# Kernel optimization log

Measured on AMD Instinct MI355X. Metric: run time of the kernel, lower is better.

The kernel has to match this reference:

```python
import jax, jax.numpy as jnp
import numpy as np

B, D_MODEL, N_LAYERS = 8, 512, 4
D_STATE, D_CONV, EXPAND, DT_RANK = 16, 4, 2, 32
D_INNER = EXPAND * D_MODEL
NUM_CLASSES = 10
ALPHA = 0.2  # observer_alpha
LN_EPS = 1e-5


def setup_inputs() -> dict:
    key = jax.random.key(0)
    ks = jax.random.split(key, 10)
    std = 0.02
    rn = lambda k, sh: (jax.random.normal(k, sh) * std).astype(jnp.float32)
    return {
        "x": jax.random.normal(ks[0], (B, 3, 32, 32), dtype=jnp.float32),
        "W_inp": rn(ks[1], (3, D_MODEL)), "b_inp": jnp.zeros((D_MODEL,), jnp.float32),
        "W_in": rn(ks[2], (N_LAYERS, D_MODEL, 2 * D_INNER)), "b_in": jnp.zeros((N_LAYERS, 2 * D_INNER), jnp.float32),
        "conv_w": rn(ks[3], (N_LAYERS, D_INNER, D_CONV)), "conv_b": jnp.zeros((N_LAYERS, D_INNER), jnp.float32),
        "W_x": rn(ks[4], (N_LAYERS, D_INNER, DT_RANK + 2 * D_STATE)),
        "W_dt": rn(ks[5], (N_LAYERS, DT_RANK, D_INNER)), "b_dt": jnp.zeros((N_LAYERS, D_INNER), jnp.float32),
        "A_log": jnp.broadcast_to(jnp.log(jnp.arange(1, D_STATE + 1, dtype=jnp.float32)), (N_LAYERS, D_INNER, D_STATE)) + 0.0,
        "D_skip": jnp.ones((N_LAYERS, D_INNER), jnp.float32),
        "W_out": rn(ks[6], (N_LAYERS, D_INNER, D_MODEL)), "b_out": jnp.zeros((N_LAYERS, D_MODEL), jnp.float32),
        "ln_w": jnp.ones((N_LAYERS, D_MODEL), jnp.float32), "ln_b": jnp.zeros((N_LAYERS, D_MODEL), jnp.float32),
        "lnf_w": jnp.ones((D_MODEL,), jnp.float32), "lnf_b": jnp.zeros((D_MODEL,), jnp.float32),
        "W_cls": rn(ks[7], (D_MODEL, NUM_CLASSES)), "b_cls": jnp.zeros((NUM_CLASSES,), jnp.float32),
    }


def layernorm(x, w, b):
    mu = x.mean(-1, keepdims=True)
    var = jnp.mean(jnp.square(x - mu), -1, keepdims=True)
    return (x - mu) * jax.lax.rsqrt(var + LN_EPS) * w + b


def mamba_layer(x, Wi, bi, cw, cb, Wx, Wdt, bdt, Alog, Dv, Wo, bo):
    # x: [B, L, d_model]
    Bsz, L, _ = x.shape
    u, z = jnp.split(x @ Wi + bi, 2, axis=-1)  # each [B, L, d_inner]
    # causal depthwise conv1d, kernel width D_CONV
    up = jnp.pad(u, ((0, 0), (D_CONV - 1, 0), (0, 0)))
    uc = cb + sum(up[:, k:k + L, :] * cw[:, k] for k in range(D_CONV))
    uc = jax.nn.silu(uc)
    dbc = uc @ Wx  # [B, L, dt_rank + 2*d_state]
    dt = jax.nn.softplus(dbc[..., :DT_RANK] @ Wdt + bdt)       # [B, L, d_inner]
    Bm = dbc[..., DT_RANK:DT_RANK + D_STATE]                    # [B, L, d_state]
    Cm = dbc[..., DT_RANK + D_STATE:]                           # [B, L, d_state]
    A = -jnp.exp(Alog)                                          # [d_inner, d_state]

    def step(h, inp):
        u_t, dt_t, B_t, C_t = inp  # [B,E],[B,E],[B,N],[B,N]
        h = jnp.exp(dt_t[..., None] * A) * h + (dt_t * u_t)[..., None] * B_t[:, None, :]
        # Luenberger observer correction: h <- h + alpha * (u - C.h) * C^T
        err = u_t - jnp.einsum('ben,bn->be', h, C_t)
        h = h + ALPHA * err[..., None] * C_t[:, None, :]
        y = jnp.einsum('ben,bn->be', h, C_t)
        return h, y

    step = jax.checkpoint(step)
    h0 = jnp.zeros((Bsz, D_INNER, D_STATE), dtype=x.dtype)
    xs = (uc.transpose(1, 0, 2), dt.transpose(1, 0, 2), Bm.transpose(1, 0, 2), Cm.transpose(1, 0, 2))
    _, ys = jax.lax.scan(step, h0, xs)
    y = ys.transpose(1, 0, 2) + Dv * uc
    y = y * jax.nn.silu(z)
    return y @ Wo + bo


def reference(x, W_inp, b_inp, W_in, b_in, conv_w, conv_b, W_x, W_dt, b_dt, A_log, D_skip, W_out, b_out, ln_w, ln_b, lnf_w, lnf_b, W_cls, b_cls):
    Bsz = x.shape[0]
    t = x.transpose(0, 2, 3, 1).reshape(Bsz, -1, 3)  # [B, H*W, 3]
    t = t @ W_inp + b_inp                             # [B, L, d_model]
    for i in range(N_LAYERS):
        t = t + mamba_layer(layernorm(t, ln_w[i], ln_b[i]), W_in[i], b_in[i], conv_w[i], conv_b[i], W_x[i], W_dt[i], b_dt[i], A_log[i], D_skip[i], W_out[i], b_out[i])
    t = t.mean(axis=1)
    t = layernorm(t, lnf_w, lnf_b)
    return t @ W_cls + b_cls
```

## Files before the change

### kernel.cpp

```cpp
#include <hip/hip_runtime.h>
#include <hip/hip_bf16.h>
#include <math.h>

#define BSZ 8
#define SEQL 1024
#define DM 512
#define DI 1024
#define DST 16
#define DTR 32
#define NLAYERS 4
#define ALPHA_C 0.2f
#define LNEPS 1e-5f
#define CH 64
#define KS64 8
#define YSTR 18

typedef __attribute__((ext_vector_type(8))) short short8;
typedef __attribute__((ext_vector_type(4))) float f32x4;

__device__ __forceinline__ void gll16(const void* g, void* l) {
    __builtin_amdgcn_global_load_lds(
        (const __attribute__((address_space(1))) unsigned int*)g,
        (__attribute__((address_space(3))) unsigned int*)l, 16, 0, 0);
}

__device__ __forceinline__ float sum16(float x) {
    x += __int_as_float(__builtin_amdgcn_update_dpp(0, __float_as_int(x), 0x121, 0xf, 0xf, true));
    x += __int_as_float(__builtin_amdgcn_update_dpp(0, __float_as_int(x), 0x122, 0xf, 0xf, true));
    x += __int_as_float(__builtin_amdgcn_update_dpp(0, __float_as_int(x), 0x124, 0xf, 0xf, true));
    x += __int_as_float(__builtin_amdgcn_update_dpp(0, __float_as_int(x), 0x128, 0xf, 0xf, true));
    return x;
}

__device__ __forceinline__ float bf2f(unsigned short v) {
    return __uint_as_float(((unsigned)v) << 16);
}

__global__ __launch_bounds__(256) void embed_kernel(const float* __restrict__ x,
                                                    const float* __restrict__ Wi,
                                                    const float* __restrict__ bi,
                                                    float* __restrict__ t) {
    int idx = blockIdx.x * 256 + threadIdx.x;
    if (idx >= BSZ * SEQL * DM) return;
    int d  = idx & (DM - 1);
    int bl = idx >> 9;
    int l  = bl & (SEQL - 1);
    int b  = bl >> 10;
    const float* xb = x + (size_t)b * 3 * SEQL;
    float acc = bi[d];
    acc += xb[0 * SEQL + l] * Wi[0 * DM + d];
    acc += xb[1 * SEQL + l] * Wi[1 * DM + d];
    acc += xb[2 * SEQL + l] * Wi[2 * DM + d];
    t[idx] = acc;
}

__global__ __launch_bounds__(256) void ln_kernel(const float* __restrict__ t,
                                                 const float* __restrict__ w,
                                                 const float* __restrict__ b,
                                                 __hip_bfloat16* __restrict__ xn) {
    int row = blockIdx.x;
    int tid = threadIdx.x;
    const float* r = t + (size_t)row * DM;
    float v0 = r[tid], v1 = r[tid + 256];
    __shared__ float sh[256], sh2[256];
    sh[tid]  = v0 + v1;
    sh2[tid] = v0 * v0 + v1 * v1;
    __syncthreads();
    for (int off = 128; off > 0; off >>= 1) {
        if (tid < off) { sh[tid] += sh[tid + off]; sh2[tid] += sh2[tid + off]; }
        __syncthreads();
    }
    float mu  = sh[0]  * (1.f / DM);
    float var = sh2[0] * (1.f / DM) - mu * mu;
    float rs  = rsqrtf(var + LNEPS);
    xn[(size_t)row * DM + tid]       = __float2bfloat16((v0 - mu) * rs * w[tid]       + b[tid]);
    xn[(size_t)row * DM + tid + 256] = __float2bfloat16((v1 - mu) * rs * w[tid + 256] + b[tid + 256]);
}

__global__ __launch_bounds__(256) void transpose_bf_kernel(const float* __restrict__ W,
                                                           __hip_bfloat16* __restrict__ Wt,
                                                           int K, int N, size_t lstride) {
    const float* Wl = W + (size_t)blockIdx.z * lstride;
    __hip_bfloat16* Wtl = Wt + (size_t)blockIdx.z * lstride;
    __shared__ float tile[32][33];
    int kk = blockIdx.x * 32, nn = blockIdx.y * 32;
    int tx = threadIdx.x & 31, ty = threadIdx.x >> 5;
#pragma unroll
    for (int i = 0; i < 32; i += 8)
        tile[ty + i][tx] = Wl[(size_t)(kk + ty + i) * N + nn + tx];
    __syncthreads();
#pragma unroll
    for (int i = 0; i < 32; i += 8)
        Wtl[(size_t)(nn + ty + i) * K + kk + tx] = __float2bfloat16(tile[tx][ty + i]);
}

template <int OUTMODE>
__global__ __launch_bounds__(256) void gemm_mfma_kernel(const short* __restrict__ A,
                                                        const short* __restrict__ Bt,
                                                        const float* __restrict__ bias,
                                                        void* __restrict__ Cv,
                                                        int M, int N, int K) {
    __shared__ __align__(16) short As[128 * 64];
    __shared__ __align__(16) short Bs[128 * 64];
    int tid = threadIdx.x;
    int w = tid >> 6, lane = tid & 63;
    int quad = lane >> 4, ml = lane & 15;
    int wm = w & 1, wn = w >> 1;
    const short* Ab = A + (size_t)blockIdx.x * 128 * K;
    const short* Bb = Bt + (size_t)blockIdx.y * 128 * K;
    f32x4 acc[4][4] = {};
    int rS[4], cS[4];
#pragma unroll
    for (int i = 0; i < 4; i++) {
        int s = i * 256 + tid;
        rS[i] = s >> 3;
        cS[i] = (s & 7) ^ (rS[i] & 7);
    }
    int aoff[2][4], boff[2][4];
#pragma unroll
    for (int kc = 0; kc < 2; kc++)
#pragma unroll
        for (int t = 0; t < 4; t++) {
            int ra = wm * 64 + t * 16 + ml;
            aoff[kc][t] = ra * 64 + ((kc * 4 + quad) ^ (ra & 7)) * 8;
            int rb = wn * 64 + t * 16 + ml;
            boff[kc][t] = rb * 64 + ((kc * 4 + quad) ^ (rb & 7)) * 8;
        }
    for (int kk = 0; kk < K; kk += 64) {
#pragma unroll
        for (int i = 0; i < 4; i++) {
            gll16(Ab + (size_t)rS[i] * K + kk + cS[i] * 8, As + (size_t)(i * 256 + w * 64) * 8);
            gll16(Bb + (size_t)rS[i] * K + kk + cS[i] * 8, Bs + (size_t)(i * 256 + w * 64) * 8);
        }
        __syncthreads();
#pragma unroll
        for (int kc = 0; kc < 2; kc++) {
            short8 af[4], bfr[4];
#pragma unroll
            for (int t = 0; t < 4; t++) af[t]  = *(const short8*)&As[aoff[kc][t]];
#pragma unroll
            for (int t = 0; t < 4; t++) bfr[t] = *(const short8*)&Bs[boff[kc][t]];
#pragma unroll
            for (int mt = 0; mt < 4; mt++)
#pragma unroll
                for (int nt = 0; nt < 4; nt++)
                    acc[mt][nt] = __builtin_amdgcn_mfma_f32_16x16x32_bf16(af[mt], bfr[nt], acc[mt][nt], 0, 0, 0);
        }
        __syncthreads();
    }
#pragma unroll
    for (int mt = 0; mt < 4; mt++) {
#pragma unroll
        for (int nt = 0; nt < 4; nt++) {
            int n = blockIdx.y * 128 + wn * 64 + nt * 16 + ml;
            float bv = bias[n];
#pragma unroll
            for (int r = 0; r < 4; r++) {
                int m = blockIdx.x * 128 + wm * 64 + mt * 16 + quad * 4 + r;
                size_t off = (size_t)m * N + n;
                float v = acc[mt][nt][r] + bv;
                if (OUTMODE == 2) {
                    ((unsigned short*)Cv)[off] = __bfloat16_as_ushort(__float2bfloat16(v));
                } else {
                    float* C = (float*)Cv;
                    if (OUTMODE == 1) v += C[off];
                    C[off] = v;
                }
            }
        }
    }
}

__global__ __launch_bounds__(256) void gemm6464_res_kernel(const short* __restrict__ A,
                                                           const short* __restrict__ Bt,
                                                           const float* __restrict__ bias,
                                                           float* __restrict__ C,
                                                           int M, int N, int K) {
    __shared__ __align__(16) short As[64 * 64];
    __shared__ __align__(16) short Bs[64 * 64];
    int tid = threadIdx.x;
    int w = tid >> 6, lane = tid & 63;
    int quad = lane >> 4, ml = lane & 15;
    int wm = w & 1, wn = w >> 1;
    const short* Ab = A + (size_t)blockIdx.x * 64 * K;
    const short* Bb = Bt + (size_t)blockIdx.y * 64 * K;
    f32x4 acc[2][2] = {};
    int rS[2], cS[2];
#pragma unroll
    for (int i = 0; i < 2; i++) {
        int s = i * 256 + tid;
        rS[i] = s >> 3;
        cS[i] = (s & 7) ^ (rS[i] & 7);
    }
    int aoff[2][2], boff[2][2];
#pragma unroll
    for (int kc = 0; kc < 2; kc++)
#pragma unroll
        for (int t = 0; t < 2; t++) {
            int ra = wm * 32 + t * 16 + ml;
            aoff[kc][t] = ra * 64 + ((kc * 4 + quad) ^ (ra & 7)) * 8;
            int rb = wn * 32 + t * 16 + ml;
            boff[kc][t] = rb * 64 + ((kc * 4 + quad) ^ (rb & 7)) * 8;
        }
    for (int kk = 0; kk < K; kk += 64) {
#pragma unroll
        for (int i = 0; i < 2; i++) {
            gll16(Ab + (size_t)rS[i] * K + kk + cS[i] * 8, As + (size_t)(i * 256 + w * 64) * 8);
            gll16(Bb + (size_t)rS[i] * K + kk + cS[i] * 8, Bs + (size_t)(i * 256 + w * 64) * 8);
        }
        __syncthreads();
#pragma unroll
        for (int kc = 0; kc < 2; kc++) {
            short8 af[2], bfr[2];
#pragma unroll
            for (int t = 0; t < 2; t++) af[t]  = *(const short8*)&As[aoff[kc][t]];
#pragma unroll
            for (int t = 0; t < 2; t++) bfr[t] = *(const short8*)&Bs[boff[kc][t]];
#pragma unroll
            for (int mt = 0; mt < 2; mt++)
#pragma unroll
                for (int nt = 0; nt < 2; nt++)
                    acc[mt][nt] = __builtin_amdgcn_mfma_f32_16x16x32_bf16(af[mt], bfr[nt], acc[mt][nt], 0, 0, 0);
        }
        __syncthreads();
    }
#pragma unroll
    for (int mt = 0; mt < 2; mt++) {
#pragma unroll
        for (int nt = 0; nt < 2; nt++) {
            int n = blockIdx.y * 64 + wn * 32 + nt * 16 + ml;
            float bv = bias[n];
#pragma unroll
            for (int r = 0; r < 4; r++) {
                int m = blockIdx.x * 64 + wm * 32 + mt * 16 + quad * 4 + r;
                size_t off = (size_t)m * N + n;
                C[off] = acc[mt][nt][r] + bv + C[off];
            }
        }
    }
}

__global__ __launch_bounds__(256) void conv_kernel(const unsigned short* __restrict__ uzb,
                                                   const float* __restrict__ cw,
                                                   const float* __restrict__ cb,
                                                   unsigned short* __restrict__ ucb) {
    int idx = blockIdx.x * 256 + threadIdx.x;
    int e  = idx & (DI - 1);
    int bl = idx >> 10;
    int l  = bl & (SEQL - 1);
    int b  = bl >> 10;
    const unsigned short* u = uzb + (size_t)b * SEQL * 2048;
    float acc = cb[e];
#pragma unroll
    for (int k = 0; k < 4; k++) {
        int ll = l - 3 + k;
        float uv = (ll >= 0) ? bf2f(u[(size_t)ll * 2048 + e]) : 0.f;
        acc += uv * cw[e * 4 + k];
    }
    acc = acc / (1.f + __expf(-acc));
    ucb[idx] = __bfloat16_as_ushort(__float2bfloat16(acc));
}

__global__ __launch_bounds__(256) void gemm64_mfma_kernel(const short* __restrict__ A,
                                                          const short* __restrict__ Bt,
                                                          float* __restrict__ part,
                                                          int M) {
    const int K = DI;
    const int Kseg = K / KS64;
    __shared__ __align__(16) short As[128 * 32];
    __shared__ __align__(16) short Bs[64 * 32];
    int tid = threadIdx.x;
    int w = tid >> 6, lane = tid & 63;
    int quad = lane >> 4, ml = lane & 15;
    int wm = w & 1, wn = w >> 1;
    int bm = blockIdx.x, ks = blockIdx.y;
    const short* Ab = A + (size_t)bm * 128 * K;
    f32x4 acc[4][2] = {};
    int s0 = tid, s1 = tid + 256;
    int r0 = s0 >> 2, c0 = (s0 & 3) ^ ((r0 >> 1) & 3);
    int r1 = s1 >> 2, c1 = (s1 & 3) ^ ((r1 >> 1) & 3);
    int rB = tid >> 2, cB = (tid & 3) ^ ((rB >> 1) & 3);
    int aoff[4], boff[2];
#pragma unroll
    for (int t = 0; t < 4; t++) {
        int ra = wm * 64 + t * 16 + ml;
        aoff[t] = ra * 32 + (quad ^ ((ra >> 1) & 3)) * 8;
    }
#pragma unroll
    for (int t = 0; t < 2; t++) {
        int rb = wn * 32 + t * 16 + ml;
        boff[t] = rb * 32 + (quad ^ ((rb >> 1) & 3)) * 8;
    }
    int k0 = ks * Kseg;
    for (int kk = k0; kk < k0 + Kseg; kk += 32) {
        gll16(Ab + (size_t)r0 * K + kk + c0 * 8, As + (size_t)(w * 64) * 8);
        gll16(Ab + (size_t)r1 * K + kk + c1 * 8, As + (size_t)(256 + w * 64) * 8);
        gll16(Bt + (size_t)rB * K + kk + cB * 8, Bs + (size_t)(w * 64) * 8);
        __syncthreads();
        short8 af[4], bfr[2];
#pragma unroll
        for (int t = 0; t < 4; t++) af[t]  = *(const short8*)&As[aoff[t]];
#pragma unroll
        for (int t = 0; t < 2; t++) bfr[t] = *(const short8*)&Bs[boff[t]];
#pragma unroll
        for (int mt = 0; mt < 4; mt++)
#pragma unroll
            for (int nt = 0; nt < 2; nt++)
                acc[mt][nt] = __builtin_amdgcn_mfma_f32_16x16x32_bf16(af[mt], bfr[nt], acc[mt][nt], 0, 0, 0);
        __syncthreads();
    }
#pragma unroll
    for (int mt = 0; mt < 4; mt++) {
#pragma unroll
        for (int nt = 0; nt < 2; nt++) {
            int n = wn * 32 + nt * 16 + ml;
#pragma unroll
            for (int r = 0; r < 4; r++) {
                int m = bm * 128 + wm * 64 + mt * 16 + quad * 4 + r;
                part[((size_t)ks * M + m) * 64 + n] = acc[mt][nt][r];
            }
        }
    }
}

__global__ __launch_bounds__(256) void dt_kernel(const float* __restrict__ part,
                                                 const float* __restrict__ Wdt,
                                                 const float* __restrict__ bdt,
                                                 const unsigned short* __restrict__ ucb,
                                                 unsigned* __restrict__ dub,
                                                 unsigned* __restrict__ bcb,
                                                 float* __restrict__ ssqb,
                                                 int M) {
    __shared__ float sdtc[32][32];
    __shared__ float swdt[32][256];
    int tid = threadIdx.x;
    int e0 = (blockIdx.x & 3) * 256;
    int m0 = (blockIdx.x >> 2) * 32;
#pragma unroll
    for (int i = 0; i < 4; i++) {
        int idx = tid + 256 * i;
        int m = idx >> 5, r = idx & 31;
        float v = 0.f;
#pragma unroll
        for (int ks = 0; ks < KS64; ks++) v += part[((size_t)ks * M + m0 + m) * 64 + r];
        sdtc[m][r] = v;
    }
    if ((blockIdx.x & 3) == 0) {
#pragma unroll
        for (int i = 0; i < 4; i++) {
            int idx = tid + 256 * i;
            int m = m0 + (idx >> 5);
            int j = idx & 31;
            float v = 0.f;
#pragma unroll
            for (int ks = 0; ks < KS64; ks++) v += part[((size_t)ks * M + m) * 64 + 32 + j];
            int n = j & 15;
            unsigned short u16 = __bfloat16_as_ushort(__float2bfloat16(v));
            unsigned short* bp = (unsigned short*)(bcb + (size_t)m * 16 + n);
            if (j < 16) {
                bp[0] = u16;
            } else {
                bp[1] = u16;
                float vr = bf2f(u16);
                float s = sum16(vr * vr);
                if (j == 16) ssqb[m] = s;
            }
        }
    }
#pragma unroll
    for (int r = 0; r < 32; r++) swdt[r][tid] = Wdt[(size_t)r * DI + e0 + tid];
    __syncthreads();
    float wc[32];
#pragma unroll
    for (int r = 0; r < 32; r++) wc[r] = swdt[r][tid];
    float bv = bdt[e0 + tid];
    for (int m = 0; m < 32; m++) {
        float acc = bv;
#pragma unroll
        for (int r4 = 0; r4 < 8; r4++) {
            float4 d4 = *(const float4*)&sdtc[m][r4 * 4];
            acc = fmaf(d4.x, wc[r4 * 4 + 0], acc);
            acc = fmaf(d4.y, wc[r4 * 4 + 1], acc);
            acc = fmaf(d4.z, wc[r4 * 4 + 2], acc);
            acc = fmaf(d4.w, wc[r4 * 4 + 3], acc);
        }
        float sp = (acc > 20.f) ? acc : log1pf(__expf(acc));
        unsigned dt16 = (unsigned)__bfloat16_as_ushort(__float2bfloat16(sp));
        unsigned u16  = (unsigned)ucb[(size_t)(m0 + m) * DI + e0 + tid];
        dub[(size_t)(m0 + m) * DI + e0 + tid] = (dt16 << 16) | u16;
    }
}

__device__ __forceinline__ void scan_stage(unsigned* sDU, unsigned* sBC,
                                           const unsigned* __restrict__ dub_row,
                                           const unsigned* __restrict__ bcb_row,
                                           int e_base, int tid, int tc) {
    int w = tid >> 6;
    int t4 = tid >> 2, c4 = tid & 3;
    gll16(dub_row + (size_t)(tc + t4) * 1024 + e_base + c4 * 4, sDU + w * 256);
    gll16(bcb_row + (size_t)(tc + t4) * 16 + c4 * 4,            sBC + w * 256);
}

__device__ __forceinline__ void scan_flush(const float* yb, __hip_bfloat16* ob,
                                           int e_base, int tcp, int tid) {
#pragma unroll
    for (int r = 0; r < 2; r++) {
        int pid = r * 256 + tid;
        int t = pid >> 3, ep = pid & 7;
        float2 y2 = *(const float2*)&yb[t * YSTR + ep * 2];
        __hip_bfloat162 v;
        v.x = __float2bfloat16(y2.x);
        v.y = __float2bfloat16(y2.y);
        *(__hip_bfloat162*)&ob[(size_t)(tcp + t) * DI + e_base + ep * 2] = v;
    }
}

__global__ __launch_bounds__(256, 2) void scan_kernel(const unsigned* __restrict__ dub,
                                                      const unsigned short* __restrict__ uzb,
                                                      const unsigned* __restrict__ bcb,
                                                      const float* __restrict__ ssqb,
                                                      const float* __restrict__ Alog,
                                                      const float* __restrict__ Dv,
                                                      __hip_bfloat16* __restrict__ out) {
    __shared__ __align__(16) unsigned sDU[2][CH * 16];
    __shared__ __align__(16) unsigned sBC[2][CH * 16];
    __shared__ __align__(16) float    yb [2][CH * YSTR];
    int tid = threadIdx.x;
    int g = tid >> 4, n = tid & 15;
    int b = blockIdx.x >> 6;
    int e_base = (blockIdx.x & 63) << 4;
    int e = e_base + g;
    float An2 = -__expf(Alog[e * DST + n]) * 1.4426950408889634f;
    float dv = Dv[e];
    const unsigned*       dub_row = dub + (size_t)b * SEQL * DI;
    const unsigned short* zP      = uzb + (size_t)b * SEQL * 2048 + 1024 + e;
    const unsigned*       bcb_row = bcb + (size_t)b * SEQL * 16;
    const float*          sqP     = ssqb + (size_t)b * SEQL;
    __hip_bfloat16* ob = out + (size_t)b * SEQL * DI;
    float h = 0.f;
    scan_stage(sDU[0], sBC[0], dub_row, bcb_row, e_base, tid, 0);
    int buf = 0;
    for (int c = 0; c < SEQL / CH; c++) {
        int tc = c * CH;
        __syncthreads();
        if (c + 1 < SEQL / CH)
            scan_stage(sDU[buf ^ 1], sBC[buf ^ 1], dub_row, bcb_row, e_base, tid, tc + CH);
        if (c > 0)
            scan_flush(yb[buf ^ 1], ob, e_base, tc - CH, tid);
        const unsigned* pDU = sDU[buf];
        const unsigned* pBC = sBC[buf];
        float* pY = yb[buf];
        for (int ts = 0; ts < CH; ts += 16) {
            unsigned du16[16], bc16[16];
#pragma unroll
            for (int j = 0; j < 16; j++) {
                du16[j] = pDU[(ts + j) * 16 + g];
                bc16[j] = pBC[(ts + j) * 16 + n];
            }
            int tl = ts + n;
            float sq = sqP[tc + tl];
            float zv = bf2f(zP[(size_t)(tc + tl) * 2048]);
            float pc = 0.f, ucap = 0.f;
#pragma unroll
            for (int j = 0; j < 16; j++) {
                unsigned du = du16[j];
                float dtv = __uint_as_float(du & 0xFFFF0000u);
                float uv  = __uint_as_float(du << 16);
                unsigned bcd = bc16[j];
                float Bn = __uint_as_float(bcd << 16);
                float Cn = __uint_as_float(bcd & 0xFFFF0000u);
                float a = __builtin_amdgcn_exp2f(dtv * An2);
                h = fmaf(a, h, dtv * uv * Bn);
                float p = sum16(h * Cn);
                h = fmaf(uv - p, ALPHA_C * Cn, h);
                bool cap = (n == j);
                pc   = cap ? p  : pc;
                ucap = cap ? uv : ucap;
            }
            float es2 = ALPHA_C * (ucap - pc);
            float y = fmaf(dv, ucap, fmaf(es2, sq, pc));
            float sz = zv / (1.f + __expf(-zv));
            pY[tl * YSTR + g] = y * sz;
        }
        buf ^= 1;
    }
    __syncthreads();
    scan_flush(yb[buf ^ 1], ob, e_base, SEQL - CH, tid);
}

__global__ __launch_bounds__(512) void pool_kernel(const float* __restrict__ t,
                                                   float* __restrict__ part) {
    int b = blockIdx.x >> 4;
    int c = blockIdx.x & 15;
    int d = threadIdx.x;
    const float* tb = t + ((size_t)b * SEQL + c * 64) * DM + d;
    float s = 0.f;
    for (int l = 0; l < 64; l++) s += tb[(size_t)l * DM];
    part[(size_t)blockIdx.x * DM + d] = s;
}

__global__ __launch_bounds__(512) void final_kernel(const float* __restrict__ part,
                                                    const float* __restrict__ lw,
                                                    const float* __restrict__ lb,
                                                    const float* __restrict__ Wc,
                                                    const float* __restrict__ bc,
                                                    float* __restrict__ out) {
    int b = blockIdx.x;
    int d = threadIdx.x;
    float v = 0.f;
    for (int c = 0; c < 16; c++) v += part[((size_t)b * 16 + c) * DM + d];
    v *= (1.f / SEQL);
    __shared__ float sh[512], sh2[512], nd[512];
    sh[d] = v; sh2[d] = v * v;
    __syncthreads();
    for (int off = 256; off > 0; off >>= 1) {
        if (d < off) { sh[d] += sh[d + off]; sh2[d] += sh2[d + off]; }
        __syncthreads();
    }
    float mu  = sh[0]  * (1.f / DM);
    float var = sh2[0] * (1.f / DM) - mu * mu;
    float rs  = rsqrtf(var + LNEPS);
    nd[d] = (v - mu) * rs * lw[d] + lb[d];
    __syncthreads();
    if (d < 10) {
        float acc = bc[d];
        for (int k = 0; k < DM; k++) acc += nd[k] * Wc[k * 10 + d];
        out[b * 10 + d] = acc;
    }
}

extern "C" void kernel_launch(void* const* d_in, const int* in_sizes, int n_in,
                              void* d_out, int out_size, void* d_ws, size_t ws_size,
                              hipStream_t stream) {
    const float* x      = (const float*)d_in[0];
    const float* W_inp  = (const float*)d_in[1];
    const float* b_inp  = (const float*)d_in[2];
    const float* W_in   = (const float*)d_in[3];
    const float* b_in   = (const float*)d_in[4];
    const float* conv_w = (const float*)d_in[5];
    const float* conv_b = (const float*)d_in[6];
    const float* W_x    = (const float*)d_in[7];
    const float* W_dt   = (const float*)d_in[8];
    const float* b_dt   = (const float*)d_in[9];
    const float* A_log  = (const float*)d_in[10];
    const float* D_skip = (const float*)d_in[11];
    const float* W_out  = (const float*)d_in[12];
    const float* b_out  = (const float*)d_in[13];
    const float* ln_w   = (const float*)d_in[14];
    const float* ln_b   = (const float*)d_in[15];
    const float* lnf_w  = (const float*)d_in[16];
    const float* lnf_b  = (const float*)d_in[17];
    const float* W_cls  = (const float*)d_in[18];
    const float* b_cls  = (const float*)d_in[19];

    const int M = BSZ * SEQL;

    float* ws = (float*)d_ws;
    float* t_buf = ws;                          ws += (size_t)M * DM;
    unsigned short* uzb = (unsigned short*)ws;  ws += (size_t)M * 2048 / 2;
    unsigned short* ucb = (unsigned short*)ws;  ws += (size_t)M * DI / 2;
    unsigned* dub  = (unsigned*)ws;             ws += (size_t)M * DI;
    unsigned* bcbu = (unsigned*)ws;             ws += (size_t)M * 16;
    float* ssqb  = ws;                          ws += (size_t)M;
    unsigned short* xn_bf = (unsigned short*)ws;  ws += (size_t)M * DM / 2;
    unsigned short* ucs_bf = (unsigned short*)ws; ws += (size_t)M * DI / 2;
    float* partb = ws;                          ws += (size_t)KS64 * M * 64;
    unsigned short* wtin_bf  = (unsigned short*)ws; ws += (size_t)NLAYERS * DM * 2048 / 2;
    unsigned short* wtout_bf = (unsigned short*)ws; ws += (size_t)NLAYERS * DI * DM / 2;
    unsigned short* wxt_bf   = (unsigned short*)ws; ws += (size_t)NLAYERS * DI * 64 / 2 + 64;
    float* poolp = ws;                          ws += (size_t)128 * DM;

    embed_kernel<<<(M * DM + 255) / 256, 256, 0, stream>>>(x, W_inp, b_inp, t_buf);
    transpose_bf_kernel<<<dim3(DM / 32, 2048 / 32, NLAYERS), 256, 0, stream>>>(
        W_in, (__hip_bfloat16*)wtin_bf, DM, 2048, (size_t)DM * 2048);
    transpose_bf_kernel<<<dim3(DI / 32, DM / 32, NLAYERS), 256, 0, stream>>>(
        W_out, (__hip_bfloat16*)wtout_bf, DI, DM, (size_t)DI * DM);
    transpose_bf_kernel<<<dim3(DI / 32, 64 / 32, NLAYERS), 256, 0, stream>>>(
        W_x, (__hip_bfloat16*)wxt_bf, DI, 64, (size_t)DI * 64);

    for (int i = 0; i < NLAYERS; i++) {
        ln_kernel<<<M, 256, 0, stream>>>(t_buf, ln_w + i * DM, ln_b + i * DM,
                                         (__hip_bfloat16*)xn_bf);
        gemm_mfma_kernel<2><<<dim3(M / 128, 2048 / 128), 256, 0, stream>>>(
            (const short*)xn_bf, (const short*)(wtin_bf + (size_t)i * DM * 2048),
            b_in + i * 2048, uzb, M, 2048, DM);
        conv_kernel<<<(M * DI) / 256, 256, 0, stream>>>(
            uzb, conv_w + (size_t)i * DI * 4, conv_b + i * DI, ucb);
        gemm64_mfma_kernel<<<dim3(M / 128, KS64), 256, 0, stream>>>(
            (const short*)ucb, (const short*)(wxt_bf + (size_t)i * DI * 64), partb, M);
        dt_kernel<<<(M / 32) * 4, 256, 0, stream>>>(
            partb, W_dt + (size_t)i * DTR * DI, b_dt + i * DI, ucb, dub, bcbu, ssqb, M);
        scan_kernel<<<BSZ * DI / 16, 256, 0, stream>>>(
            dub, uzb, bcbu, ssqb, A_log + (size_t)i * DI * DST, D_skip + i * DI,
            (__hip_bfloat16*)ucs_bf);
        gemm6464_res_kernel<<<dim3(M / 64, DM / 64), 256, 0, stream>>>(
            (const short*)ucs_bf, (const short*)(wtout_bf + (size_t)i * DI * DM),
            b_out + i * DM, t_buf, M, DM, DI);
    }

    pool_kernel<<<128, 512, 0, stream>>>(t_buf, poolp);
    final_kernel<<<8, 512, 0, stream>>>(poolp, lnf_w, lnf_b, W_cls, b_cls, (float*)d_out);
}
```

Baseline: 1.147 ms.

## Transpose dt/u and B/C buffers to time-major per channel for vectorized scan loads

The dt kernel now writes the packed dt/u and B/C values transposed, so each channel's (or state's) time series is contiguous. The scan kernel then loads them with register-staged uint4 global loads into padded shared rows instead of global_load_lds. It also reads four timesteps per uint4 from shared memory with software prefetch, replacing sixteen scalar reads. The cost is that the dt kernel's column writes become strided across channels, which may hurt its store coalescing.

New measurement: 1.387 ms. 1.21x slower.

```diff
diff --git a/kernel.cpp b/kernel.cpp
--- a/kernel.cpp
+++ b/kernel.cpp
@@ -14,6 +14,7 @@
 #define CH 64
 #define KS64 8
 #define YSTR 18
+#define SROW 68
 
 typedef __attribute__((ext_vector_type(8))) short short8;
 typedef __attribute__((ext_vector_type(4))) float f32x4;
@@ -327,8 +328,8 @@
                                                  const float* __restrict__ Wdt,
                                                  const float* __restrict__ bdt,
                                                  const unsigned short* __restrict__ ucb,
-                                                 unsigned* __restrict__ dub,
-                                                 unsigned* __restrict__ bcb,
+                                                 unsigned* __restrict__ dub_t,
+                                                 unsigned* __restrict__ bcb_t,
                                                  float* __restrict__ ssqb,
                                                  int M) {
     __shared__ float sdtc[32][32];
@@ -336,6 +337,8 @@
     int tid = threadIdx.x;
     int e0 = (blockIdx.x & 3) * 256;
     int m0 = (blockIdx.x >> 2) * 32;
+    int mb = m0 >> 10;
+    int t0 = m0 & 1023;
 #pragma unroll
     for (int i = 0; i < 4; i++) {
         int idx = tid + 256 * i;
@@ -355,8 +358,9 @@
 #pragma unroll
             for (int ks = 0; ks < KS64; ks++) v += part[((size_t)ks * M + m) * 64 + 32 + j];
             int n = j & 15;
+            int tt = m & 1023;
             unsigned short u16 = __bfloat16_as_ushort(__float2bfloat16(v));
-            unsigned short* bp = (unsigned short*)(bcb + (size_t)m * 16 + n);
+            unsigned short* bp = (unsigned short*)(bcb_t + ((size_t)mb * 16 + n) * SEQL + tt);
             if (j < 16) {
                 bp[0] = u16;
             } else {
@@ -374,6 +378,7 @@
 #pragma unroll
     for (int r = 0; r < 32; r++) wc[r] = swdt[r][tid];
     float bv = bdt[e0 + tid];
+    unsigned* dcol = dub_t + ((size_t)mb * DI + e0 + tid) * SEQL + t0;
     for (int m = 0; m < 32; m++) {
         float acc = bv;
 #pragma unroll
@@ -387,18 +392,8 @@
         float sp = (acc > 20.f) ? acc : log1pf(__expf(acc));
         unsigned dt16 = (unsigned)__bfloat16_as_ushort(__float2bfloat16(sp));
         unsigned u16  = (unsigned)ucb[(size_t)(m0 + m) * DI + e0 + tid];
-        dub[(size_t)(m0 + m) * DI + e0 + tid] = (dt16 << 16) | u16;
-    }
-}
-
-__device__ __forceinline__ void scan_stage(unsigned* sDU, unsigned* sBC,
-                                           const unsigned* __restrict__ dub_row,
-                                           const unsigned* __restrict__ bcb_row,
-                                           int e_base, int tid, int tc) {
-    int w = tid >> 6;
-    int t4 = tid >> 2, c4 = tid & 3;
-    gll16(dub_row + (size_t)(tc + t4) * 1024 + e_base + c4 * 4, sDU + w * 256);
-    gll16(bcb_row + (size_t)(tc + t4) * 16 + c4 * 4,            sBC + w * 256);
+        dcol[m] = (dt16 << 16) | u16;
+    }
 }
 
 __device__ __forceinline__ void scan_flush(const float* yb, __hip_bfloat16* ob,
@@ -415,15 +410,15 @@
     }
 }
 
-__global__ __launch_bounds__(256, 2) void scan_kernel(const unsigned* __restrict__ dub,
+__global__ __launch_bounds__(256, 2) void scan_kernel(const unsigned* __restrict__ dub_t,
                                                       const unsigned short* __restrict__ uzb,
-                                                      const unsigned* __restrict__ bcb,
+                                                      const unsigned* __restrict__ bcb_t,
                                                       const float* __restrict__ ssqb,
                                                       const float* __restrict__ Alog,
                                                       const float* __restrict__ Dv,
                                                       __hip_bfloat16* __restrict__ out) {
-    __shared__ __align__(16) unsigned sDU[2][CH * 16];
-    __shared__ __align__(16) unsigned sBC[2][CH * 16];
+    __shared__ __align__(16) unsigned sDU[2][16 * SROW];
+    __shared__ __align__(16) unsigned sBC[2][16 * SROW];
     __shared__ __align__(16) float    yb [2][CH * YSTR];
     int tid = threadIdx.x;
     int g = tid >> 4, n = tid & 15;
@@ -432,55 +427,82 @@
     int e = e_base + g;
     float An2 = -__expf(Alog[e * DST + n]) * 1.4426950408889634f;
     float dv = Dv[e];
-    const unsigned*       dub_row = dub + (size_t)b * SEQL * DI;
-    const unsigned short* zP      = uzb + (size_t)b * SEQL * 2048 + 1024 + e;
-    const unsigned*       bcb_row = bcb + (size_t)b * SEQL * 16;
-    const float*          sqP     = ssqb + (size_t)b * SEQL;
+    int er = tid >> 4, tq = (tid & 15) * 4;
+    const unsigned* duRow = dub_t + ((size_t)b * DI + e_base + er) * SEQL + tq;
+    const unsigned* bcRow = bcb_t + ((size_t)b * 16 + er) * SEQL + tq;
+    int dst = er * SROW + tq;
+    const unsigned short* zP  = uzb + (size_t)b * SEQL * 2048 + 1024 + e;
+    const float*          sqP = ssqb + (size_t)b * SEQL;
     __hip_bfloat16* ob = out + (size_t)b * SEQL * DI;
     float h = 0.f;
-    scan_stage(sDU[0], sBC[0], dub_row, bcb_row, e_base, tid, 0);
+    {
+        uint4 a = *(const uint4*)(duRow);
+        uint4 c = *(const uint4*)(bcRow);
+        *(uint4*)&sDU[0][dst] = a;
+        *(uint4*)&sBC[0][dst] = c;
+    }
     int buf = 0;
-    for (int c = 0; c < SEQL / CH; c++) {
+    const int NCH = SEQL / CH;
+    for (int c = 0; c < NCH; c++) {
         int tc = c * CH;
         __syncthreads();
-        if (c + 1 < SEQL / CH)
-            scan_stage(sDU[buf ^ 1], sBC[buf ^ 1], dub_row, bcb_row, e_base, tid, tc + CH);
+        uint4 gdu, gbc;
+        bool more = (c + 1 < NCH);
+        if (more) {
+            gdu = *(const uint4*)(duRow + tc + CH);
+            gbc = *(const uint4*)(bcRow + tc + CH);
+        }
         if (c > 0)
             scan_flush(yb[buf ^ 1], ob, e_base, tc - CH, tid);
-        const unsigned* pDU = sDU[buf];
-        const unsigned* pBC = sBC[buf];
+        const unsigned* pDU = &sDU[buf][g * SROW];
+        const unsigned* pBC = &sBC[buf][n * SROW];
         float* pY = yb[buf];
-        for (int ts = 0; ts < CH; ts += 16) {
-            unsigned du16[16], bc16[16];
-#pragma unroll
-            for (int j = 0; j < 16; j++) {
-                du16[j] = pDU[(ts + j) * 16 + g];
-                bc16[j] = pBC[(ts + j) * 16 + n];
-            }
-            int tl = ts + n;
-            float sq = sqP[tc + tl];
-            float zv = bf2f(zP[(size_t)(tc + tl) * 2048]);
-            float pc = 0.f, ucap = 0.f;
-#pragma unroll
-            for (int j = 0; j < 16; j++) {
-                unsigned du = du16[j];
+        uint4 du4 = *(const uint4*)&pDU[0];
+        uint4 bc4 = *(const uint4*)&pBC[0];
+        float pc = 0.f, ucap = 0.f, sq = 0.f, zv = 0.f;
+#pragma unroll
+        for (int p = 0; p < 16; p++) {
+            uint4 duN, bcN;
+            if (p < 15) {
+                duN = *(const uint4*)&pDU[(p + 1) * 4];
+                bcN = *(const uint4*)&pBC[(p + 1) * 4];
+            }
+            if ((p & 3) == 0) {
+                int tl = (p >> 2) * 16 + n;
+                sq = sqP[tc + tl];
+                zv = bf2f(zP[(size_t)(tc + tl) * 2048]);
+                pc = 0.f; ucap = 0.f;
+            }
+            unsigned dus[4] = {du4.x, du4.y, du4.z, du4.w};
+            unsigned bcs[4] = {bc4.x, bc4.y, bc4.z, bc4.w};
+#pragma unroll
+            for (int j = 0; j < 4; j++) {
+                unsigned du = dus[j];
                 float dtv = __uint_as_float(du & 0xFFFF0000u);
                 float uv  = __uint_as_float(du << 16);
-                unsigned bcd = bc16[j];
+                unsigned bcd = bcs[j];
                 float Bn = __uint_as_float(bcd << 16);
                 float Cn = __uint_as_float(bcd & 0xFFFF0000u);
                 float a = __builtin_amdgcn_exp2f(dtv * An2);
                 h = fmaf(a, h, dtv * uv * Bn);
-                float p = sum16(h * Cn);
-                h = fmaf(uv - p, ALPHA_C * Cn, h);
-                bool cap = (n == j);
-                pc   = cap ? p  : pc;
+                float p2 = sum16(h * Cn);
+                h = fmaf(uv - p2, ALPHA_C * Cn, h);
+                bool cap = (n == ((p & 3) * 4 + j));
+                pc   = cap ? p2 : pc;
                 ucap = cap ? uv : ucap;
             }
-            float es2 = ALPHA_C * (ucap - pc);
-            float y = fmaf(dv, ucap, fmaf(es2, sq, pc));
-            float sz = zv / (1.f + __expf(-zv));
-            pY[tl * YSTR + g] = y * sz;
+            if ((p & 3) == 3) {
+                int tl = (p >> 2) * 16 + n;
+                float es2 = ALPHA_C * (ucap - pc);
+                float y = fmaf(dv, ucap, fmaf(es2, sq, pc));
+                float sz = zv / (1.f + __expf(-zv));
+                pY[tl * YSTR + g] = y * sz;
+            }
+            du4 = duN; bc4 = bcN;
+        }
+        if (more) {
+            *(uint4*)&sDU[buf ^ 1][dst] = gdu;
+            *(uint4*)&sBC[buf ^ 1][dst] = gbc;
         }
         buf ^= 1;
     }
@@ -559,8 +581,8 @@
     float* t_buf = ws;                          ws += (size_t)M * DM;
     unsigned short* uzb = (unsigned short*)ws;  ws += (size_t)M * 2048 / 2;
     unsigned short* ucb = (unsigned short*)ws;  ws += (size_t)M * DI / 2;
-    unsigned* dub  = (unsigned*)ws;             ws += (size_t)M * DI;
-    unsigned* bcbu = (unsigned*)ws;             ws += (size_t)M * 16;
+    unsigned* dub_t = (unsigned*)ws;            ws += (size_t)M * DI;
+    unsigned* bcb_t = (unsigned*)ws;            ws += (size_t)BSZ * 16 * SEQL;
     float* ssqb  = ws;                          ws += (size_t)M;
     unsigned short* xn_bf = (unsigned short*)ws;  ws += (size_t)M * DM / 2;
     unsigned short* ucs_bf = (unsigned short*)ws; ws += (size_t)M * DI / 2;
@@ -589,9 +611,9 @@
         gemm64_mfma_kernel<<<dim3(M / 128, KS64), 256, 0, stream>>>(
             (const short*)ucb, (const short*)(wxt_bf + (size_t)i * DI * 64), partb, M);
         dt_kernel<<<(M / 32) * 4, 256, 0, stream>>>(
-            partb, W_dt + (size_t)i * DTR * DI, b_dt + i * DI, ucb, dub, bcbu, ssqb, M);
+            partb, W_dt + (size_t)i * DTR * DI, b_dt + i * DI, ucb, dub_t, bcb_t, ssqb, M);
         scan_kernel<<<BSZ * DI / 16, 256, 0, stream>>>(
-            dub, uzb, bcbu, ssqb, A_log + (size_t)i * DI * DST, D_skip + i * DI,
+            dub_t, uzb, bcb_t, ssqb, A_log + (size_t)i * DI * DST, D_skip + i * DI,
             (__hip_bfloat16*)ucs_bf);
         gemm6464_res_kernel<<<dim3(M / 64, DM / 64), 256, 0, stream>>>(
             (const short*)ucs_bf, (const short*)(wtout_bf + (size_t)i * DI * DM),
```
